# Kernel optimization log

Measured on AMD Instinct MI355X. Metric: run time of the kernel, lower is better.

Reference implementation:

```python
import jax, jax.numpy as jnp
import numpy as np

MIN_NORM = 1e-15
PROJ_EPS = 4e-3  # float32 boundary eps used by hgcn PoincareBall.proj
C = 1.0          # curvature for every layer
N, E, D = 10000, 320000, 256


def _norm(x):
    return jnp.maximum(jnp.linalg.norm(x, axis=-1, keepdims=True), MIN_NORM)


def artanh(x):
    return jnp.arctanh(jnp.clip(x, -1 + 1e-7, 1 - 1e-7))


def proj(x, c):
    norm = _norm(x)
    maxnorm = (1.0 - PROJ_EPS) / jnp.sqrt(c)
    return jnp.where(norm > maxnorm, x / norm * maxnorm, x)


def expmap0(u, c):
    sqrt_c = jnp.sqrt(c)
    u_norm = _norm(u)
    return jnp.tanh(sqrt_c * u_norm) * u / (sqrt_c * u_norm)


def logmap0(p, c):
    sqrt_c = jnp.sqrt(c)
    p_norm = _norm(p)
    return artanh(sqrt_c * p_norm) * p / (sqrt_c * p_norm)


def mobius_add(x, y, c):
    x2 = jnp.sum(x * x, -1, keepdims=True)
    y2 = jnp.sum(y * y, -1, keepdims=True)
    xy = jnp.sum(x * y, -1, keepdims=True)
    num = (1 + 2 * c * xy + c * y2) * x + (1 - c * x2) * y
    denom = 1 + 2 * c * xy + c * c * x2 * y2
    return num / jnp.maximum(denom, MIN_NORM)


def mobius_matvec(m, x, c):
    sqrt_c = jnp.sqrt(c)
    x_norm = _norm(x)
    mx = x @ m.T
    mx_norm = _norm(mx)
    res = jnp.tanh(mx_norm / x_norm * artanh(sqrt_c * x_norm)) * mx / (mx_norm * sqrt_c)
    zero_row = jnp.all(mx == 0, axis=-1, keepdims=True)
    return jnp.where(zero_row, jnp.zeros_like(res), res)


def hgc_layer(h, W, b, edge_weight, edge_src, edge_dst, c):
    # HypLinear (dropout=0, eval mode)
    res = proj(mobius_matvec(W, h, c), c)
    hyp_bias = proj(expmap0(b[None, :], c), c)
    h = proj(mobius_add(res, hyp_bias, c), c)
    # HypAgg: tangent-space neighborhood aggregation (spmm over edge list)
    xt = logmap0(h, c)                                  # [N, D]
    msgs = edge_weight[:, None] * xt[edge_src]          # [E, D] irregular gather
    agg = jax.ops.segment_sum(msgs, edge_dst, num_segments=N)
    h = proj(expmap0(agg, c), c)
    # HypAct: relu in tangent space, map back with c_out
    xt = jax.nn.relu(logmap0(h, c))
    return proj(expmap0(xt, c), c)


def setup_inputs() -> dict:
    key = jax.random.key(0)
    ks = jax.random.split(key, 8)
    x = jax.random.normal(ks[0], (N, D), dtype=jnp.float32)
    edge_src = jax.random.randint(ks[1], (E,), 0, N)
    edge_dst = jax.random.randint(ks[2], (E,), 0, N)
    # normalized-adjacency-like positive weights (~1/deg scale)
    edge_weight = jax.random.uniform(ks[3], (E,), dtype=jnp.float32) / 32.0
    s = 1.0 / np.sqrt(D)
    W1 = jax.random.normal(ks[4], (D, D), dtype=jnp.float32) * s
    b1 = jnp.zeros((D,), dtype=jnp.float32)
    W2 = jax.random.normal(ks[5], (D, D), dtype=jnp.float32) * s
    b2 = jnp.zeros((D,), dtype=jnp.float32)
    return {"x": x, "W1": W1, "b1": b1, "W2": W2, "b2": b2,
            "edge_weight": edge_weight, "edge_src": edge_src, "edge_dst": edge_dst}


def reference(x, W1, b1, W2, b2, edge_weight, edge_src, edge_dst):
    # old=True path: map Euclidean features onto the Poincare ball first
    h = proj(expmap0(x, C), C)
    h = hgc_layer(h, W1, b1, edge_weight, edge_src, edge_dst, C)
    h = hgc_layer(h, W2, b2, edge_weight, edge_src, edge_dst, C)
    return h
```

## Files before the change

### kernel.cpp

```cpp
#include <hip/hip_runtime.h>
#include <hip/hip_fp16.h>

#define DIM 256
#define MAXNORM 0.996f
#define MINN 1e-15f
#define CLIPV 0.9999999f

typedef __attribute__((ext_vector_type(8))) short bf16x8;
typedef __attribute__((ext_vector_type(4))) float f32x4;

__device__ __forceinline__ unsigned short f2bf(float f) {
    unsigned int u = __float_as_uint(f);
    u += 0x7fffu + ((u >> 16) & 1u);
    return (unsigned short)(u >> 16);
}
__device__ __forceinline__ float h2f(unsigned short h) {
    return __half2float(__ushort_as_half(h));
}
__device__ __forceinline__ unsigned short f2h(float f) {
    return __half_as_ushort(__float2half(f));
}
__device__ __forceinline__ float wsum(float v) {
    v += __shfl_xor(v, 32);
    v += __shfl_xor(v, 16);
    v += __shfl_xor(v, 8);
    v += __shfl_xor(v, 4);
    v += __shfl_xor(v, 2);
    v += __shfl_xor(v, 1);
    return v;
}
__device__ __forceinline__ float gsum16(float v) {
    v += __shfl_xor(v, 8);
    v += __shfl_xor(v, 4);
    v += __shfl_xor(v, 2);
    v += __shfl_xor(v, 1);
    return v;
}

__global__ void k_setup(const float* __restrict__ x, unsigned short* __restrict__ h_bf,
                        float* __restrict__ hnorm2, int nrows,
                        int* __restrict__ csr_off, int nOff,
                        const float* __restrict__ W1, const float* __restrict__ W2,
                        unsigned short* __restrict__ w_bf, int nPerW, int eB) {
    int bid = blockIdx.x;
    if (bid < eB) {
        int gid = bid * 256 + threadIdx.x;
        int row = gid >> 6, lane = gid & 63;
        if (row >= nrows) return;
        size_t base = (size_t)row * DIM + lane * 4;
        float4 v = *(const float4*)(x + base);
        float ss = wsum(v.x * v.x + v.y * v.y + v.z * v.z + v.w * v.w);
        float n = fmaxf(sqrtf(ss), MINN);
        float tn = tanhf(n);
        float hn = (tn > MAXNORM) ? MAXNORM : tn;
        float s = hn / n;
        ushort4 ob;
        ob.x = f2bf(v.x * s); ob.y = f2bf(v.y * s);
        ob.z = f2bf(v.z * s); ob.w = f2bf(v.w * s);
        *(ushort4*)(h_bf + base) = ob;
        if (lane == 0) hnorm2[row] = hn * hn;
    } else if (bid < eB + 64) {
        int i = (bid - eB) * 256 + threadIdx.x;
        int stride = 64 * 256;
        for (; i < nOff; i += stride) csr_off[i] = 0;
    } else {
        int i = (bid - eB - 64) * 256 + threadIdx.x;
        int stride = 128 * 256;
        for (; i < 2 * nPerW; i += stride)
            w_bf[i] = f2bf(i < nPerW ? W1[i] : W2[i - nPerW]);
    }
}

__global__ void k_hist(const int* __restrict__ dst, int* __restrict__ off, int nE, int nrows) {
    int e = blockIdx.x * blockDim.x + threadIdx.x;
    if (e >= nE) return;
    int d = dst[e];
    if (d >= 0 && d < nrows) atomicAdd(&off[d + 1], 1);
}

__global__ void k_scan(int* __restrict__ a, int* __restrict__ cursor, int n) {
    __shared__ int wsums[16];
    int t = threadIdx.x;
    int chunk = (n + 1023) / 1024;
    int lo = t * chunk, hi = min(lo + chunk, n);
    int sum = 0;
    for (int i = lo; i < hi; ++i) sum += a[i];
    int lane = t & 63, wid = t >> 6;
    int v = sum;
    for (int o = 1; o < 64; o <<= 1) {
        int u = __shfl_up(v, o);
        if (lane >= o) v += u;
    }
    if (lane == 63) wsums[wid] = v;
    __syncthreads();
    if (t == 0) {
        int c = 0;
        for (int i = 0; i < 16; ++i) { int x = wsums[i]; wsums[i] = c; c += x; }
    }
    __syncthreads();
    int excl = v - sum + wsums[wid];
    int c = excl;
    for (int i = lo; i < hi; ++i) {
        c += a[i];
        a[i] = c;
        if (i < n - 1) cursor[i] = c;
    }
}

__global__ void k_fill(const int* __restrict__ esrc, const int* __restrict__ edst,
                       const float* __restrict__ ew, int* __restrict__ cursor,
                       int2* __restrict__ csr_pack, int nE, int nrows) {
    int e = blockIdx.x * blockDim.x + threadIdx.x;
    if (e >= nE) return;
    int d = edst[e];
    if (d < 0 || d >= nrows) return;
    int pos = atomicAdd(&cursor[d], 1);
    csr_pack[pos] = make_int2(esrc[e], __float_as_int(ew[e]));
}

__global__ void k_gemm_post(const unsigned short* __restrict__ Abf,
                            const unsigned short* __restrict__ Wbf,
                            const float* __restrict__ hnorm2,
                            const float* __restrict__ bias,
                            unsigned short* __restrict__ XT, int M) {
    int wave = threadIdx.x >> 6;
    int lane = threadIdx.x & 63;
    int r = lane & 15, oct = lane >> 4;
    int i0 = (blockIdx.x * 4 + wave) * 16;
    int arow = i0 + r;
    bool av = arow < M;
    const unsigned short* ap = Abf + (size_t)(av ? arow : 0) * DIM + oct * 8;
    const unsigned short* wp = Wbf + (size_t)r * DIM + oct * 8;
    const bf16x8 zf = {0, 0, 0, 0, 0, 0, 0, 0};
    f32x4 acc[16];
#pragma unroll
    for (int jt = 0; jt < 16; ++jt) acc[jt] = (f32x4){0.f, 0.f, 0.f, 0.f};
    for (int k0 = 0; k0 < 256; k0 += 32) {
        bf16x8 a = av ? *(const bf16x8*)(ap + k0) : zf;
#pragma unroll
        for (int jt = 0; jt < 16; ++jt) {
            bf16x8 w = *(const bf16x8*)(wp + (size_t)jt * 16 * DIM + k0);
            acc[jt] = __builtin_amdgcn_mfma_f32_16x16x32_bf16(a, w, acc[jt], 0, 0, 0);
        }
    }
    float bv[16];
    float bss = 0.f;
#pragma unroll
    for (int jt = 0; jt < 16; ++jt) {
        bv[jt] = bias[jt * 16 + r];
        bss = fmaf(bv[jt], bv[jt], bss);
    }
    bss = gsum16(bss);
    float bn = fmaxf(sqrtf(bss), MINN);
    float btn = tanhf(bn);
    float bhn = (btn > MAXNORM) ? MAXNORM : btn;
    float bscale = bhn / bn;
    float y2 = bhn * bhn;
#pragma unroll
    for (int jt = 0; jt < 16; ++jt) bv[jt] *= bscale;

#pragma unroll
    for (int q = 0; q < 4; ++q) {
        int row = i0 + oct * 4 + q;
        float sm = 0.f, sxy = 0.f;
#pragma unroll
        for (int jt = 0; jt < 16; ++jt) {
            float m = acc[jt][q];
            sm  = fmaf(m, m, sm);
            sxy = fmaf(m, bv[jt], sxy);
        }
        sm = gsum16(sm);
        sxy = gsum16(sxy);
        if (row < M) {
            float sh = hnorm2[row];
            float xn = fmaxf(sqrtf(sh), MINN);
            float at = atanhf(fminf(xn, CLIPV));
            float mn = fmaxf(sqrtf(sm), MINN);
            float t = tanhf(mn / xn * at);
            float alpha = t / mn;
            float resn = t;
            if (t > MAXNORM) { alpha = MAXNORM / mn; resn = MAXNORM; }
            float x2 = resn * resn;
            float xy = alpha * sxy;
            float Aa = 1.f + 2.f * xy + y2;
            float Bb = 1.f - x2;
            float den = fmaxf(1.f + 2.f * xy + x2 * y2, MINN);
            float s_m = Aa * alpha / den;
            float s_b = Bb / den;
            float hn2 = (Aa * Aa * x2 + 2.f * Aa * Bb * xy + Bb * Bb * y2) / (den * den);
            float hn = fmaxf(sqrtf(fmaxf(hn2, 0.f)), MINN);
            if (hn > MAXNORM) { float f = MAXNORM / hn; s_m *= f; s_b *= f; hn = MAXNORM; }
            float lt = atanhf(fminf(hn, CLIPV)) / hn;
            s_m *= lt; s_b *= lt;
#pragma unroll
            for (int jt = 0; jt < 16; ++jt)
                XT[(size_t)row * DIM + jt * 16 + r] = f2h(fmaf(s_m, acc[jt][q], s_b * bv[jt]));
        }
    }
}

__global__ void k_agg_finish(const unsigned short* __restrict__ XT, const int* __restrict__ off,
                             const int2* __restrict__ cpk,
                             float* __restrict__ OUT, unsigned short* __restrict__ OUT_bf,
                             float* __restrict__ hnorm2, int nrows) {
    int gid = blockIdx.x * blockDim.x + threadIdx.x;
    int row = gid >> 6, lane = gid & 63;
    if (row >= nrows) return;
    int p0 = off[row], p1 = off[row + 1];
    float a0 = 0.f, a1 = 0.f, a2 = 0.f, a3 = 0.f;
    int p = p0;
    for (; p + 7 < p1; p += 8) {
        ushort4 v[8];
        float w[8];
#pragma unroll
        for (int u = 0; u < 8; ++u) {
            int2 pk = cpk[p + u];
            w[u] = __int_as_float(pk.y);
            v[u] = *(const ushort4*)(XT + (size_t)pk.x * DIM + lane * 4);
        }
#pragma unroll
        for (int u = 0; u < 8; ++u) {
            a0 = fmaf(w[u], h2f(v[u].x), a0);
            a1 = fmaf(w[u], h2f(v[u].y), a1);
            a2 = fmaf(w[u], h2f(v[u].z), a2);
            a3 = fmaf(w[u], h2f(v[u].w), a3);
        }
    }
    for (; p < p1; ++p) {
        int2 pk = cpk[p];
        float w = __int_as_float(pk.y);
        ushort4 v = *(const ushort4*)(XT + (size_t)pk.x * DIM + lane * 4);
        a0 = fmaf(w, h2f(v.x), a0); a1 = fmaf(w, h2f(v.y), a1);
        a2 = fmaf(w, h2f(v.z), a2); a3 = fmaf(w, h2f(v.w), a3);
    }
    float ss = wsum(a0 * a0 + a1 * a1 + a2 * a2 + a3 * a3);
    float n = fmaxf(sqrtf(ss), MINN);
    float tn = tanhf(n);
    float hn = (tn > MAXNORM) ? MAXNORM : tn;
    float s1 = hn / n;
    float lt = atanhf(fminf(hn, CLIPV)) / fmaxf(hn, MINN);
    float s2 = lt * s1;
    float x0 = fmaxf(s2 * a0, 0.f), x1 = fmaxf(s2 * a1, 0.f);
    float x2 = fmaxf(s2 * a2, 0.f), x3 = fmaxf(s2 * a3, 0.f);
    float ss2 = wsum(x0 * x0 + x1 * x1 + x2 * x2 + x3 * x3);
    float n2 = fmaxf(sqrtf(ss2), MINN);
    float tn2 = tanhf(n2);
    float hn2c = (tn2 > MAXNORM) ? MAXNORM : tn2;
    float s3 = hn2c / n2;
    float o0 = s3 * x0, o1 = s3 * x1, o2 = s3 * x2, o3 = s3 * x3;
    size_t base = (size_t)row * DIM + lane * 4;
    if (OUT_bf) {
        ushort4 ob;
        ob.x = f2bf(o0); ob.y = f2bf(o1); ob.z = f2bf(o2); ob.w = f2bf(o3);
        *(ushort4*)(OUT_bf + base) = ob;
        if (lane == 0) hnorm2[row] = hn2c * hn2c;
    } else {
        *(float4*)(OUT + base) = make_float4(o0, o1, o2, o3);
    }
}

static inline size_t align256(size_t x) { return (x + 255) & ~(size_t)255; }

extern "C" void kernel_launch(void* const* d_in, const int* in_sizes, int n_in,
                              void* d_out, int out_size, void* d_ws, size_t ws_size,
                              hipStream_t stream) {
    const float* x  = (const float*)d_in[0];
    const float* W1 = (const float*)d_in[1];
    const float* b1 = (const float*)d_in[2];
    const float* W2 = (const float*)d_in[3];
    const float* b2 = (const float*)d_in[4];
    const float* ew = (const float*)d_in[5];
    const int* esrc = (const int*)d_in[6];
    const int* edst = (const int*)d_in[7];
    const int nE = in_sizes[5];
    const int M  = in_sizes[0] / DIM;

    size_t S = (size_t)M * DIM;
    char* base = (char*)d_ws;
    size_t o = 0;
    int2* csr_pack = (int2*)(base + o);          o = align256(o + (size_t)nE * 8);
    int* csr_off   = (int*)(base + o);           o = align256(o + (size_t)(M + 1) * 4);
    int* cursor    = (int*)(base + o);           o = align256(o + (size_t)M * 4);
    float* hnorm2  = (float*)(base + o);         o = align256(o + (size_t)(M + 64) * 4);
    unsigned short* xt   = (unsigned short*)(base + o);  o = align256(o + S * 2);
    unsigned short* h_bf = (unsigned short*)(base + o);  o = align256(o + S * 2);
    unsigned short* w_bf = (unsigned short*)(base + o);  o = align256(o + (size_t)2 * DIM * DIM * 2);

    int rowBlocks = (M + 3) / 4;
    int edgeBlocks = (nE + 255) / 256;

    k_setup<<<rowBlocks + 64 + 128, 256, 0, stream>>>(
        x, h_bf, hnorm2, M, csr_off, M + 1, W1, W2, w_bf, DIM * DIM, rowBlocks);

    k_hist<<<edgeBlocks, 256, 0, stream>>>(edst, csr_off, nE, M);
    k_scan<<<1, 1024, 0, stream>>>(csr_off, cursor, M + 1);
    k_fill<<<edgeBlocks, 256, 0, stream>>>(esrc, edst, ew, cursor, csr_pack, nE, M);

    for (int layer = 0; layer < 2; ++layer) {
        const float* b = (layer == 0) ? b1 : b2;
        const unsigned short* Wb = w_bf + (size_t)layer * DIM * DIM;
        k_gemm_post<<<(M + 63) / 64, 256, 0, stream>>>(h_bf, Wb, hnorm2, b, xt, M);
        k_agg_finish<<<rowBlocks, 256, 0, stream>>>(
            xt, csr_off, csr_pack,
            (layer == 0) ? (float*)nullptr : (float*)d_out,
            (layer == 0) ? h_bf : (unsigned short*)nullptr,
            hnorm2, M);
    }
}
```

Before: 230.1 us.

## Split GEMM output columns across waves with LDS reduction of row norms

Each block now handles 16 rows, and each of its four waves computes a quarter of the 256 output columns instead of each wave computing all 256 columns for its own 16 rows. Per-row partial sums of squared norm and dot with bias are reduced across waves through shared memory and a block barrier. This cuts per-thread accumulator registers from 64 to 16 and quadruples the block count, aiming for higher occupancy and more parallelism over the roughly 157 blocks previously launched. In exchange it adds a __syncthreads, LDS traffic, and redundant A-row loads across the four waves.

```diff
diff --git a/kernel.cpp b/kernel.cpp
--- a/kernel.cpp
+++ b/kernel.cpp
@@ -118,37 +118,41 @@
     csr_pack[pos] = make_int2(esrc[e], __float_as_int(ew[e]));
 }
 
-__global__ void k_gemm_post(const unsigned short* __restrict__ Abf,
+__global__ void __launch_bounds__(256) k_gemm_post(
+                            const unsigned short* __restrict__ Abf,
                             const unsigned short* __restrict__ Wbf,
                             const float* __restrict__ hnorm2,
                             const float* __restrict__ bias,
                             unsigned short* __restrict__ XT, int M) {
+    __shared__ float lds_sm[4][16];
+    __shared__ float lds_sxy[4][16];
     int wave = threadIdx.x >> 6;
     int lane = threadIdx.x & 63;
     int r = lane & 15, oct = lane >> 4;
-    int i0 = (blockIdx.x * 4 + wave) * 16;
+    int i0 = blockIdx.x * 16;
     int arow = i0 + r;
     bool av = arow < M;
+    int jtbase = wave * 4;
     const unsigned short* ap = Abf + (size_t)(av ? arow : 0) * DIM + oct * 8;
-    const unsigned short* wp = Wbf + (size_t)r * DIM + oct * 8;
+    const unsigned short* wp = Wbf + (size_t)(jtbase * 16 + r) * DIM + oct * 8;
     const bf16x8 zf = {0, 0, 0, 0, 0, 0, 0, 0};
-    f32x4 acc[16];
-#pragma unroll
-    for (int jt = 0; jt < 16; ++jt) acc[jt] = (f32x4){0.f, 0.f, 0.f, 0.f};
+    f32x4 acc[4];
+#pragma unroll
+    for (int j = 0; j < 4; ++j) acc[j] = (f32x4){0.f, 0.f, 0.f, 0.f};
+#pragma unroll
     for (int k0 = 0; k0 < 256; k0 += 32) {
         bf16x8 a = av ? *(const bf16x8*)(ap + k0) : zf;
 #pragma unroll
-        for (int jt = 0; jt < 16; ++jt) {
-            bf16x8 w = *(const bf16x8*)(wp + (size_t)jt * 16 * DIM + k0);
-            acc[jt] = __builtin_amdgcn_mfma_f32_16x16x32_bf16(a, w, acc[jt], 0, 0, 0);
-        }
-    }
-    float bv[16];
+        for (int j = 0; j < 4; ++j) {
+            bf16x8 w = *(const bf16x8*)(wp + (size_t)j * 16 * DIM + k0);
+            acc[j] = __builtin_amdgcn_mfma_f32_16x16x32_bf16(a, w, acc[j], 0, 0, 0);
+        }
+    }
     float bss = 0.f;
 #pragma unroll
     for (int jt = 0; jt < 16; ++jt) {
-        bv[jt] = bias[jt * 16 + r];
-        bss = fmaf(bv[jt], bv[jt], bss);
+        float b = bias[jt * 16 + r];
+        bss = fmaf(b, b, bss);
     }
     bss = gsum16(bss);
     float bn = fmaxf(sqrtf(bss), MINN);
@@ -156,21 +160,33 @@
     float bhn = (btn > MAXNORM) ? MAXNORM : btn;
     float bscale = bhn / bn;
     float y2 = bhn * bhn;
-#pragma unroll
-    for (int jt = 0; jt < 16; ++jt) bv[jt] *= bscale;
+    float bvw[4];
+#pragma unroll
+    for (int j = 0; j < 4; ++j) bvw[j] = bias[(jtbase + j) * 16 + r] * bscale;
 
 #pragma unroll
     for (int q = 0; q < 4; ++q) {
-        int row = i0 + oct * 4 + q;
         float sm = 0.f, sxy = 0.f;
 #pragma unroll
-        for (int jt = 0; jt < 16; ++jt) {
-            float m = acc[jt][q];
+        for (int j = 0; j < 4; ++j) {
+            float m = acc[j][q];
             sm  = fmaf(m, m, sm);
-            sxy = fmaf(m, bv[jt], sxy);
+            sxy = fmaf(m, bvw[j], sxy);
         }
         sm = gsum16(sm);
         sxy = gsum16(sxy);
+        if (r == 0) {
+            lds_sm[wave][oct * 4 + q] = sm;
+            lds_sxy[wave][oct * 4 + q] = sxy;
+        }
+    }
+    __syncthreads();
+#pragma unroll
+    for (int q = 0; q < 4; ++q) {
+        int row16 = oct * 4 + q;
+        int row = i0 + row16;
+        float sm  = lds_sm[0][row16] + lds_sm[1][row16] + lds_sm[2][row16] + lds_sm[3][row16];
+        float sxy = lds_sxy[0][row16] + lds_sxy[1][row16] + lds_sxy[2][row16] + lds_sxy[3][row16];
         if (row < M) {
             float sh = hnorm2[row];
             float xn = fmaxf(sqrtf(sh), MINN);
@@ -193,8 +209,9 @@
             float lt = atanhf(fminf(hn, CLIPV)) / hn;
             s_m *= lt; s_b *= lt;
 #pragma unroll
-            for (int jt = 0; jt < 16; ++jt)
-                XT[(size_t)row * DIM + jt * 16 + r] = f2h(fmaf(s_m, acc[jt][q], s_b * bv[jt]));
+            for (int j = 0; j < 4; ++j)
+                XT[(size_t)row * DIM + (jtbase + j) * 16 + r] =
+                    f2h(fmaf(s_m, acc[j][q], s_b * bvw[j]));
         }
     }
 }
@@ -299,7 +316,7 @@
     for (int layer = 0; layer < 2; ++layer) {
         const float* b = (layer == 0) ? b1 : b2;
         const unsigned short* Wb = w_bf + (size_t)layer * DIM * DIM;
-        k_gemm_post<<<(M + 63) / 64, 256, 0, stream>>>(h_bf, Wb, hnorm2, b, xt, M);
+        k_gemm_post<<<(M + 15) / 16, 256, 0, stream>>>(h_bf, Wb, hnorm2, b, xt, M);
         k_agg_finish<<<rowBlocks, 256, 0, stream>>>(
             xt, csr_off, csr_pack,
             (layer == 0) ? (float*)nullptr : (float*)d_out,
```

Result: no change. 233.5 us (+1.5%).
